# Kernel optimization log

Hardware: AMD Instinct MI355X
Metric: run time of the kernel (lower is better)

## Reference

```python
import jax, jax.numpy as jnp
import numpy as np

N = 65536      # total atoms
D = 1024       # hidden_size (encoder output dim)
H = 2048       # ffn_hidden_size
OUT = 1        # output_size
M = 4096       # number of molecules (segments)


def _lin(k, fi, fo):
    return jax.random.normal(k, (fi, fo), jnp.float32) * (1.0 / np.sqrt(fi))


def setup_inputs() -> dict:
    key = jax.random.key(0)
    ks = jax.random.split(key, 14)
    hidden = jax.random.normal(ks[0], (N, D), jnp.float32)
    segment_ids = jnp.sort(jax.random.randint(ks[1], (N,), 0, M)).astype(jnp.int64)
    inp = {
        "hidden": hidden,
        "ffn_W1": _lin(ks[2], D, H), "ffn_b1": jnp.zeros((H,), jnp.float32),
        "ffn_W2": _lin(ks[3], H, H), "ffn_b2": jnp.zeros((H,), jnp.float32),
        "ffn_W3": _lin(ks[4], H, OUT), "ffn_b3": jnp.zeros((OUT,), jnp.float32),
        "wr_W1": _lin(ks[5], D, H), "wr_b1": jnp.zeros((H,), jnp.float32),
        "wr_W2": _lin(ks[6], H, H), "wr_b2": jnp.zeros((H,), jnp.float32),
        "wr_W3": _lin(ks[7], H, OUT), "wr_b3": jnp.ones((OUT,), jnp.float32),  # bias=1 keeps segment weight sums away from 0
        "segment_ids": segment_ids,
    }
    return inp


def _ffn(x, W1, b1, W2, b2, W3, b3):
    # Dropout(p) is identity in eval; activation = ReLU
    h = jax.nn.relu(x @ W1 + b1)
    h = jax.nn.relu(h @ W2 + b2)
    return h @ W3 + b3


def reference(hidden, ffn_W1, ffn_b1, ffn_W2, ffn_b2, ffn_W3, ffn_b3,
              wr_W1, wr_b1, wr_W2, wr_b2, wr_W3, wr_b3, segment_ids):
    seg = segment_ids.astype(jnp.int32)
    output = _ffn(hidden, ffn_W1, ffn_b1, ffn_W2, ffn_b2, ffn_W3, ffn_b3)   # [N, OUT]
    weights = _ffn(hidden, wr_W1, wr_b1, wr_W2, wr_b2, wr_W3, wr_b3)        # [N, OUT]
    # per-molecule sums over ALL elements of the segment slice (matches .sum())
    out_sum = jax.ops.segment_sum(output.sum(-1), seg, num_segments=M)      # [M]
    w_sum = jax.ops.segment_sum(weights.sum(-1), seg, num_segments=M)       # [M]
    ratio = (out_sum / w_sum)[seg][:, None]                                 # [N, 1]
    return output - weights * ratio
```

## Files before the change

### kernel.cpp

```cpp
#include <hip/hip_runtime.h>
#include <hip/hip_bf16.h>

#define DEVINL __device__ __forceinline__

typedef __attribute__((ext_vector_type(8))) short s8v;
typedef __attribute__((ext_vector_type(4))) float f4v;

using bf16 = __hip_bfloat16;
typedef unsigned short u16;

DEVINL u16 f2bu(float f) {
  bf16 h = __float2bfloat16(f);
  return *reinterpret_cast<u16*>(&h);
}

DEVINL void gload16(const void* g, void* l) {
  __builtin_amdgcn_global_load_lds((const __attribute__((address_space(1))) void*)g,
                                   (__attribute__((address_space(3))) void*)l, 16, 0, 0);
}

#define BAR()    __builtin_amdgcn_s_barrier()
#define LGKM(n)  asm volatile("s_waitcnt lgkmcnt(" #n ")" ::: "memory")
#define VM(n)    asm volatile("s_waitcnt vmcnt(" #n ")" ::: "memory")

__global__ void k_f32_to_bf16(const float* __restrict__ x, u16* __restrict__ y, long n4) {
  long i = (long)blockIdx.x * blockDim.x + threadIdx.x;
  if (i >= n4) return;
  float4 v = ((const float4*)x)[i];
  ushort4 o;
  o.x = f2bu(v.x); o.y = f2bu(v.y); o.z = f2bu(v.z); o.w = f2bu(v.w);
  ((ushort4*)y)[i] = o;
}

__global__ void k_transpose_bf16(const float* __restrict__ W, u16* __restrict__ Wt,
                                 int rows, int cols) {
  __shared__ float tile[32][33];
  const int tx = threadIdx.x, ty = threadIdx.y;
  const int c0 = blockIdx.x * 32, r0 = blockIdx.y * 32;
  #pragma unroll
  for (int i = ty; i < 32; i += 8)
    tile[i][tx] = W[(long)(r0 + i) * cols + (c0 + tx)];
  __syncthreads();
  #pragma unroll
  for (int i = ty; i < 32; i += 8)
    Wt[(long)(c0 + i) * rows + (r0 + tx)] = f2bu(tile[tx][i]);
}

extern __shared__ char smem[];

template<int EPI, int NT>
__global__ __launch_bounds__(512, 2)
void k_gemm8(const u16* __restrict__ A, const u16* __restrict__ Bt,
             u16* __restrict__ C, const float* __restrict__ bias,
             const float* __restrict__ w3, float* __restrict__ oacc,
             int N, int K) {
  const int tid = threadIdx.x;
  const int w = tid >> 6, lane = tid & 63;
  const int id = blockIdx.x;
  const int cpx = gridDim.x >> 3;
  const int sw = (id & 7) * cpx + (id >> 3);
  const int bn = sw & 7, bm = sw >> 3;

  const int wm = (w >> 2) * 128, wn = (w & 3) * 64;

  f4v acc[8][4];
  #pragma unroll
  for (int i = 0; i < 8; ++i)
    #pragma unroll
    for (int jj = 0; jj < 4; ++jj)
      #pragma unroll
      for (int r = 0; r < 4; ++r) acc[i][jj][r] = 0.f;

  const int rowl = tid >> 2;
  const int jsw = (tid & 3) ^ ((rowl >> 1) & 3);
  const u16* gA = A + (long)(bm * 256 + rowl) * K + jsw * 8;
  const u16* gB = Bt + (long)(bn * 256 + rowl) * K + jsw * 8;
  const long cstr = (long)128 * K;
  const uint wb = (uint)w * 1024u;

  const uint swz = ((uint)((lane >> 4) ^ ((lane >> 1) & 3))) * 16u;
  const uint aoff = (uint)(wm + (lane & 15)) * 64u + swz;
  const uint boff = (uint)(wn + (lane & 15)) * 64u + swz + 32768u;

#define STAGE_A(pp, ks, rel) do { \
    const u16* g_ = gA + (rel) * 64 + (ks) * 32; \
    char* l_ = smem + (uint)(pp) * 65536u + (uint)(ks) * 16384u + wb; \
    gload16(g_, l_); gload16(g_ + cstr, l_ + 8192); } while (0)
#define STAGE_B(pp, ks, rel) do { \
    const u16* g_ = gB + (rel) * 64 + (ks) * 32; \
    char* l_ = smem + (uint)(pp) * 65536u + 32768u + (uint)(ks) * 16384u + wb; \
    gload16(g_, l_); gload16(g_ + cstr, l_ + 8192); } while (0)

#define RD_A(dst, pbc, ksb) do { \
    _Pragma("unroll") \
    for (int mi_ = 0; mi_ < 8; ++mi_) \
      dst[mi_] = *(const s8v*)(smem + (pbc) + (ksb) + aoff + (uint)mi_ * 1024u); } while (0)
#define RD_B(dst, pbc, ksb, c0) do { \
    dst[0] = *(const s8v*)(smem + (pbc) + (ksb) + boff + (uint)(c0) * 1024u); \
    dst[1] = *(const s8v*)(smem + (pbc) + (ksb) + boff + (uint)((c0) + 1) * 1024u); } while (0)

#define MFMA8(A_, B_, c0i, c1i) do { \
    __builtin_amdgcn_s_setprio(1); \
    _Pragma("unroll") \
    for (int mi_ = 0; mi_ < 8; ++mi_) { \
      acc[mi_][c0i] = __builtin_amdgcn_mfma_f32_16x16x32_bf16(A_[mi_], B_[0], acc[mi_][c0i], 0, 0, 0); \
      acc[mi_][c1i] = __builtin_amdgcn_mfma_f32_16x16x32_bf16(A_[mi_], B_[1], acc[mi_][c1i], 0, 0, 0); \
    } \
    __builtin_amdgcn_s_setprio(0); } while (0)

#define TILE(P, REL1, REL2, S1, S2, R1) do { \
     \
    RD_B(b23, (P) * 65536u, 0u, 2); \
    if (S1) STAGE_A(1 - (P), 1, REL1); \
    BAR(); LGKM(2); \
    MFMA8(a0, b01, 0, 1); \
     \
    if (S1) { VM(6); } else { VM(0); } \
    BAR(); \
    RD_A(a1, (P) * 65536u, 16384u); RD_B(b01, (P) * 65536u, 16384u, 0); \
    if (S1) STAGE_B(1 - (P), 1, REL1); \
    LGKM(10); \
    MFMA8(a0, b23, 2, 3); \
     \
    RD_B(b23, (P) * 65536u, 16384u, 2); \
    if (S2) STAGE_A((P), 0, REL2); \
    BAR(); LGKM(2); \
    MFMA8(a1, b01, 0, 1); \
     \
    if (S2) { \
      STAGE_B((P), 0, REL2); \
      VM(8); BAR(); \
      RD_A(a0, (1 - (P)) * 65536u, 0u); RD_B(b01, (1 - (P)) * 65536u, 0u, 0); \
      LGKM(10); \
    } else if (R1) { \
      VM(4); BAR(); \
      RD_A(a0, (1 - (P)) * 65536u, 0u); RD_B(b01, (1 - (P)) * 65536u, 0u, 0); \
      LGKM(10); \
    } else { \
      BAR(); LGKM(0); \
    } \
    MFMA8(a1, b23, 2, 3); \
  } while (0)

  s8v a0[8], a1[8], b01[2], b23[2];

  STAGE_A(0, 0, 0); STAGE_B(0, 0, 0); STAGE_A(0, 1, 0); STAGE_B(0, 1, 0);
  STAGE_A(1, 0, 1); STAGE_B(1, 0, 1);
  VM(8); BAR();
  RD_A(a0, 0u, 0u); RD_B(b01, 0u, 0u, 0);

  #pragma unroll 1
  for (int tp = 0; tp < NT / 2 - 1; ++tp) {
    TILE(0, 1, 2, 1, 1, 1);
    TILE(1, 2, 3, 1, 1, 1);
    gA += 128; gB += 128;
  }
  TILE(0, 1, 2, 1, 0, 1);
  TILE(1, 2, 3, 0, 0, 0);

  const int crow = bm * 256 + wm + ((lane >> 4) << 2);
  const int ccol = bn * 256 + wn + (lane & 15);
  if (EPI == 1) {
    #pragma unroll
    for (int jj = 0; jj < 4; ++jj) {
      const float bb = bias[ccol + jj * 16];
      #pragma unroll
      for (int mi = 0; mi < 8; ++mi)
        #pragma unroll
        for (int r = 0; r < 4; ++r) {
          float v = acc[mi][jj][r] + bb;
          v = v > 0.f ? v : 0.f;
          C[(long)(crow + mi * 16 + r) * N + ccol + jj * 16] = f2bu(v);
        }
    }
  } else {
    float bb[4], ww[4];
    #pragma unroll
    for (int jj = 0; jj < 4; ++jj) { bb[jj] = bias[ccol + jj * 16]; ww[jj] = w3[ccol + jj * 16]; }
    #pragma unroll
    for (int mi = 0; mi < 8; ++mi)
      #pragma unroll
      for (int r = 0; r < 4; ++r) {
        float s = 0.f;
        #pragma unroll
        for (int jj = 0; jj < 4; ++jj) {
          float v = acc[mi][jj][r] + bb[jj];
          v = v > 0.f ? v : 0.f;
          s += v * ww[jj];
        }
        s += __shfl_xor(s, 1, 64);
        s += __shfl_xor(s, 2, 64);
        s += __shfl_xor(s, 4, 64);
        s += __shfl_xor(s, 8, 64);
        if ((lane & 15) == 0) atomicAdd(&oacc[crow + mi * 16 + r], s);
      }
  }
#undef STAGE_A
#undef STAGE_B
#undef RD_A
#undef RD_B
#undef MFMA8
#undef TILE
}

__global__ void k_detect(const int* __restrict__ seg, int n, int* __restrict__ flag) {
  if (blockIdx.x == 0 && threadIdx.x == 0) flag[0] = (seg[n - 1] == 0) ? 1 : 0;
}

__global__ void k_segsum(const float* __restrict__ oacc, const float* __restrict__ wacc,
                         const int* __restrict__ seg, const int* __restrict__ flag,
                         const float* __restrict__ ob3, const float* __restrict__ wb3,
                         float* __restrict__ osum, float* __restrict__ wsum, int n) {
  int i = blockIdx.x * blockDim.x + threadIdx.x;
  if (i >= n) return;
  int s = flag[0] ? seg[2 * i] : seg[i];
  atomicAdd(&osum[s], oacc[i] + ob3[0]);
  atomicAdd(&wsum[s], wacc[i] + wb3[0]);
}

__global__ void k_final(const float* __restrict__ oacc, const float* __restrict__ wacc,
                        const int* __restrict__ seg, const int* __restrict__ flag,
                        const float* __restrict__ ob3, const float* __restrict__ wb3,
                        const float* __restrict__ osum, const float* __restrict__ wsum,
                        float* __restrict__ out, int n) {
  int i = blockIdx.x * blockDim.x + threadIdx.x;
  if (i >= n) return;
  int s = flag[0] ? seg[2 * i] : seg[i];
  float o = oacc[i] + ob3[0];
  float ww = wacc[i] + wb3[0];
  out[i] = o - ww * (osum[s] / wsum[s]);
}

extern "C" void kernel_launch(void* const* d_in, const int* in_sizes, int n_in,
                              void* d_out, int out_size, void* d_ws, size_t ws_size,
                              hipStream_t stream) {
  constexpr int NA = 65536, D = 1024, H = 2048, M = 4096;
  const float* hidden = (const float*)d_in[0];
  const float* fW1 = (const float*)d_in[1];
  const float* fb1 = (const float*)d_in[2];
  const float* fW2 = (const float*)d_in[3];
  const float* fb2 = (const float*)d_in[4];
  const float* fW3 = (const float*)d_in[5];
  const float* fb3 = (const float*)d_in[6];
  const float* wW1 = (const float*)d_in[7];
  const float* wb1 = (const float*)d_in[8];
  const float* wW2 = (const float*)d_in[9];
  const float* wb2 = (const float*)d_in[10];
  const float* wW3 = (const float*)d_in[11];
  const float* wb3 = (const float*)d_in[12];
  const int* seg = (const int*)d_in[13];
  float* out = (float*)d_out;

  char* ws = (char*)d_ws;
  size_t off = 0;
  auto alloc = [&](size_t bytes) { char* p = ws + off; off += (bytes + 255) & ~(size_t)255; return p; };
  u16* hbf  = (u16*)alloc((size_t)NA * D * 2);
  u16* w1tf = (u16*)alloc((size_t)H * D * 2);
  u16* w1tw = (u16*)alloc((size_t)H * D * 2);
  u16* w2tf = (u16*)alloc((size_t)H * H * 2);
  u16* w2tw = (u16*)alloc((size_t)H * H * 2);
  u16* h1   = (u16*)alloc((size_t)NA * H * 2);
  float* oacc = (float*)alloc((size_t)NA * 4);
  float* wacc = (float*)alloc((size_t)NA * 4);
  float* osum = (float*)alloc((size_t)M * 4);
  float* wsum = (float*)alloc((size_t)M * 4);
  int* flag = (int*)alloc(256);

  hipFuncSetAttribute((const void*)k_gemm8<1, 16>, hipFuncAttributeMaxDynamicSharedMemorySize, 131072);
  hipFuncSetAttribute((const void*)k_gemm8<2, 32>, hipFuncAttributeMaxDynamicSharedMemorySize, 131072);

  k_f32_to_bf16<<<(int)((long)NA * D / 4 / 256), 256, 0, stream>>>(hidden, hbf, (long)NA * D / 4);
  dim3 tb(32, 8);
  k_transpose_bf16<<<dim3(H / 32, D / 32), tb, 0, stream>>>(fW1, w1tf, D, H);
  k_transpose_bf16<<<dim3(H / 32, D / 32), tb, 0, stream>>>(wW1, w1tw, D, H);
  k_transpose_bf16<<<dim3(H / 32, H / 32), tb, 0, stream>>>(fW2, w2tf, H, H);
  k_transpose_bf16<<<dim3(H / 32, H / 32), tb, 0, stream>>>(wW2, w2tw, H, H);

  hipMemsetAsync(oacc, 0, (size_t)((char*)flag - (char*)oacc), stream);
  k_detect<<<1, 64, 0, stream>>>(seg, NA, flag);

  const int nblk = (H / 256) * (NA / 256);
  k_gemm8<1, 16><<<nblk, 512, 131072, stream>>>(hbf, w1tf, h1, fb1, nullptr, nullptr, H, D);
  k_gemm8<2, 32><<<nblk, 512, 131072, stream>>>(h1, w2tf, nullptr, fb2, fW3, oacc, H, H);
  k_gemm8<1, 16><<<nblk, 512, 131072, stream>>>(hbf, w1tw, h1, wb1, nullptr, nullptr, H, D);
  k_gemm8<2, 32><<<nblk, 512, 131072, stream>>>(h1, w2tw, nullptr, wb2, wW3, wacc, H, H);

  k_segsum<<<NA / 256, 256, 0, stream>>>(oacc, wacc, seg, flag, fb3, wb3, osum, wsum, NA);
  k_final<<<NA / 256, 256, 0, stream>>>(oacc, wacc, seg, flag, fb3, wb3, osum, wsum, out, NA);
}
```

Measured before the change: 1.919 ms.

## Switch GEMM inner loop to 32x32x16 bf16 MFMA with new LDS fragment layout

Replaces the 16x16x32 MFMA tiling with 32x32x16 MFMAs, so each wave holds 4x2 accumulators of 16 floats instead of 8x4 of 4. The LDS read pattern and swizzle offsets are rebuilt for 32-row fragments, and some barriers in the pipelined tile schedule are dropped. The epilogues are remapped to the 32x32 output layout, and the row reduction gains an extra shuffle. The aim is fewer MFMA issues and fewer LDS fragment reads per FLOP, at the cost of a different pipeline and barrier schedule that may race or stall.

```diff
diff --git a/kernel.cpp b/kernel.cpp
--- a/kernel.cpp
+++ b/kernel.cpp
@@ -4,7 +4,7 @@
 #define DEVINL __device__ __forceinline__
 
 typedef __attribute__((ext_vector_type(8))) short s8v;
-typedef __attribute__((ext_vector_type(4))) float f4v;
+typedef __attribute__((ext_vector_type(16))) float f16v;
 
 using bf16 = __hip_bfloat16;
 typedef unsigned short u16;
@@ -63,13 +63,13 @@
 
   const int wm = (w >> 2) * 128, wn = (w & 3) * 64;
 
-  f4v acc[8][4];
-  #pragma unroll
-  for (int i = 0; i < 8; ++i)
-    #pragma unroll
-    for (int jj = 0; jj < 4; ++jj)
+  f16v acc[4][2];
+  #pragma unroll
+  for (int mi = 0; mi < 4; ++mi)
+    #pragma unroll
+    for (int ni = 0; ni < 2; ++ni)
       #pragma unroll
-      for (int r = 0; r < 4; ++r) acc[i][jj][r] = 0.f;
+      for (int r = 0; r < 16; ++r) acc[mi][ni][r] = 0.f;
 
   const int rowl = tid >> 2;
   const int jsw = (tid & 3) ^ ((rowl >> 1) & 3);
@@ -78,9 +78,14 @@
   const long cstr = (long)128 * K;
   const uint wb = (uint)w * 1024u;
 
-  const uint swz = ((uint)((lane >> 4) ^ ((lane >> 1) & 3))) * 16u;
-  const uint aoff = (uint)(wm + (lane & 15)) * 64u + swz;
-  const uint boff = (uint)(wn + (lane & 15)) * 64u + swz + 32768u;
+  const uint arow = (uint)(wm + (lane & 31)) * 64u;
+  const uint brow = (uint)(wn + (lane & 31)) * 64u + 32768u;
+  const uint hi = (uint)((lane >> 5) & 1);
+  const uint xw = (uint)((lane >> 1) & 3);
+  uint sl[4];
+  #pragma unroll
+  for (int s = 0; s < 4; ++s)
+    sl[s] = (((uint)(2 * (s & 1)) + hi) ^ xw) * 16u + (uint)(s >> 1) * 16384u;
 
 #define STAGE_A(pp, ks, rel) do { \
     const u16* g_ = gA + (rel) * 64 + (ks) * 32; \
@@ -91,63 +96,63 @@
     char* l_ = smem + (uint)(pp) * 65536u + 32768u + (uint)(ks) * 16384u + wb; \
     gload16(g_, l_); gload16(g_ + cstr, l_ + 8192); } while (0)
 
-#define RD_A(dst, pbc, ksb) do { \
-    _Pragma("unroll") \
-    for (int mi_ = 0; mi_ < 8; ++mi_) \
-      dst[mi_] = *(const s8v*)(smem + (pbc) + (ksb) + aoff + (uint)mi_ * 1024u); } while (0)
-#define RD_B(dst, pbc, ksb, c0) do { \
-    dst[0] = *(const s8v*)(smem + (pbc) + (ksb) + boff + (uint)(c0) * 1024u); \
-    dst[1] = *(const s8v*)(smem + (pbc) + (ksb) + boff + (uint)((c0) + 1) * 1024u); } while (0)
-
-#define MFMA8(A_, B_, c0i, c1i) do { \
+#define RD6(aD, bD, pbc, s) do { \
+    aD[0] = *(const s8v*)(smem + (pbc) + arow + sl[s]); \
+    aD[1] = *(const s8v*)(smem + (pbc) + arow + sl[s] + 2048u); \
+    aD[2] = *(const s8v*)(smem + (pbc) + arow + sl[s] + 4096u); \
+    aD[3] = *(const s8v*)(smem + (pbc) + arow + sl[s] + 6144u); \
+    bD[0] = *(const s8v*)(smem + (pbc) + brow + sl[s]); \
+    bD[1] = *(const s8v*)(smem + (pbc) + brow + sl[s] + 2048u); } while (0)
+
+#define MFMA8(aS, bS) do { \
     __builtin_amdgcn_s_setprio(1); \
     _Pragma("unroll") \
-    for (int mi_ = 0; mi_ < 8; ++mi_) { \
-      acc[mi_][c0i] = __builtin_amdgcn_mfma_f32_16x16x32_bf16(A_[mi_], B_[0], acc[mi_][c0i], 0, 0, 0); \
-      acc[mi_][c1i] = __builtin_amdgcn_mfma_f32_16x16x32_bf16(A_[mi_], B_[1], acc[mi_][c1i], 0, 0, 0); \
+    for (int mi_ = 0; mi_ < 4; ++mi_) { \
+      acc[mi_][0] = __builtin_amdgcn_mfma_f32_32x32x16_bf16(aS[mi_], bS[0], acc[mi_][0], 0, 0, 0); \
+      acc[mi_][1] = __builtin_amdgcn_mfma_f32_32x32x16_bf16(aS[mi_], bS[1], acc[mi_][1], 0, 0, 0); \
     } \
     __builtin_amdgcn_s_setprio(0); } while (0)
 
 #define TILE(P, REL1, REL2, S1, S2, R1) do { \
      \
-    RD_B(b23, (P) * 65536u, 0u, 2); \
+    RD6(aY, bY, (P) * 65536u, 1); \
     if (S1) STAGE_A(1 - (P), 1, REL1); \
-    BAR(); LGKM(2); \
-    MFMA8(a0, b01, 0, 1); \
+    LGKM(6); \
+    MFMA8(aX, bX); \
      \
     if (S1) { VM(6); } else { VM(0); } \
     BAR(); \
-    RD_A(a1, (P) * 65536u, 16384u); RD_B(b01, (P) * 65536u, 16384u, 0); \
+    RD6(aX, bX, (P) * 65536u, 2); \
     if (S1) STAGE_B(1 - (P), 1, REL1); \
-    LGKM(10); \
-    MFMA8(a0, b23, 2, 3); \
-     \
-    RD_B(b23, (P) * 65536u, 16384u, 2); \
+    LGKM(6); \
+    MFMA8(aY, bY); \
+     \
+    RD6(aY, bY, (P) * 65536u, 3); \
     if (S2) STAGE_A((P), 0, REL2); \
-    BAR(); LGKM(2); \
-    MFMA8(a1, b01, 0, 1); \
+    LGKM(6); \
+    MFMA8(aX, bX); \
      \
     if (S2) { \
+      VM(6); BAR(); \
+      RD6(aX, bX, (1 - (P)) * 65536u, 0); \
       STAGE_B((P), 0, REL2); \
-      VM(8); BAR(); \
-      RD_A(a0, (1 - (P)) * 65536u, 0u); RD_B(b01, (1 - (P)) * 65536u, 0u, 0); \
-      LGKM(10); \
+      LGKM(6); \
     } else if (R1) { \
       VM(4); BAR(); \
-      RD_A(a0, (1 - (P)) * 65536u, 0u); RD_B(b01, (1 - (P)) * 65536u, 0u, 0); \
-      LGKM(10); \
+      RD6(aX, bX, (1 - (P)) * 65536u, 0); \
+      LGKM(6); \
     } else { \
-      BAR(); LGKM(0); \
+      LGKM(0); \
     } \
-    MFMA8(a1, b23, 2, 3); \
+    MFMA8(aY, bY); \
   } while (0)
 
-  s8v a0[8], a1[8], b01[2], b23[2];
+  s8v aX[4], aY[4], bX[2], bY[2];
 
   STAGE_A(0, 0, 0); STAGE_B(0, 0, 0); STAGE_A(0, 1, 0); STAGE_B(0, 1, 0);
   STAGE_A(1, 0, 1); STAGE_B(1, 0, 1);
   VM(8); BAR();
-  RD_A(a0, 0u, 0u); RD_B(b01, 0u, 0u, 0);
+  RD6(aX, bX, 0u, 0);
 
   #pragma unroll 1
   for (int tp = 0; tp < NT / 2 - 1; ++tp) {
@@ -158,47 +163,50 @@
   TILE(0, 1, 2, 1, 0, 1);
   TILE(1, 2, 3, 0, 0, 0);
 
-  const int crow = bm * 256 + wm + ((lane >> 4) << 2);
-  const int ccol = bn * 256 + wn + (lane & 15);
+  const int colb = bn * 256 + wn + (lane & 31);
+  const int rowb = bm * 256 + wm + 4 * ((lane >> 5) & 1);
   if (EPI == 1) {
     #pragma unroll
-    for (int jj = 0; jj < 4; ++jj) {
-      const float bb = bias[ccol + jj * 16];
+    for (int ni = 0; ni < 2; ++ni) {
+      const int col = colb + ni * 32;
+      const float bb = bias[col];
       #pragma unroll
-      for (int mi = 0; mi < 8; ++mi)
+      for (int mi = 0; mi < 4; ++mi)
         #pragma unroll
-        for (int r = 0; r < 4; ++r) {
-          float v = acc[mi][jj][r] + bb;
+        for (int r = 0; r < 16; ++r) {
+          const int row = rowb + mi * 32 + (r & 3) + 8 * (r >> 2);
+          float v = acc[mi][ni][r] + bb;
           v = v > 0.f ? v : 0.f;
-          C[(long)(crow + mi * 16 + r) * N + ccol + jj * 16] = f2bu(v);
+          C[(long)row * N + col] = f2bu(v);
         }
     }
   } else {
-    float bb[4], ww[4];
-    #pragma unroll
-    for (int jj = 0; jj < 4; ++jj) { bb[jj] = bias[ccol + jj * 16]; ww[jj] = w3[ccol + jj * 16]; }
-    #pragma unroll
-    for (int mi = 0; mi < 8; ++mi)
+    float bb[2], ww[2];
+    #pragma unroll
+    for (int ni = 0; ni < 2; ++ni) { bb[ni] = bias[colb + ni * 32]; ww[ni] = w3[colb + ni * 32]; }
+    #pragma unroll
+    for (int mi = 0; mi < 4; ++mi)
       #pragma unroll
-      for (int r = 0; r < 4; ++r) {
+      for (int r = 0; r < 16; ++r) {
         float s = 0.f;
         #pragma unroll
-        for (int jj = 0; jj < 4; ++jj) {
-          float v = acc[mi][jj][r] + bb[jj];
+        for (int ni = 0; ni < 2; ++ni) {
+          float v = acc[mi][ni][r] + bb[ni];
           v = v > 0.f ? v : 0.f;
-          s += v * ww[jj];
+          s += v * ww[ni];
         }
         s += __shfl_xor(s, 1, 64);
         s += __shfl_xor(s, 2, 64);
         s += __shfl_xor(s, 4, 64);
         s += __shfl_xor(s, 8, 64);
-        if ((lane & 15) == 0) atomicAdd(&oacc[crow + mi * 16 + r], s);
+        s += __shfl_xor(s, 16, 64);
+        if ((lane & 31) == 0)
+          atomicAdd(&oacc[rowb + mi * 32 + (r & 3) + 8 * (r >> 2)], s);
       }
   }
 #undef STAGE_A
 #undef STAGE_B
-#undef RD_A
-#undef RD_B
+#undef RD6
 #undef MFMA8
 #undef TILE
 }
```

After: 2.312 ms. 20.4% more time.

## Load GEMM B fragments directly from global into registers, drop B LDS staging

Applied to the files above, without the earlier changes.

The GEMM kernel no longer stages the weight (B) tiles through shared memory. Each lane loads its B MFMA fragments straight from global memory into registers, double-buffered across k-steps, while A stays staged in LDS. This halves LDS usage to 64KB, which could allow more blocks per CU, and removes LDS traffic for B. The cost is uncoalesced, redundant global/L2 reads of B (each wave fetches its own 64 columns) and a reworked vmcnt schedule that has to cover both the B register loads and the A LDS loads.

```diff
diff --git a/kernel.cpp b/kernel.cpp
--- a/kernel.cpp
+++ b/kernel.cpp
@@ -20,7 +20,6 @@
 }
 
 #define BAR()    __builtin_amdgcn_s_barrier()
-#define LGKM(n)  asm volatile("s_waitcnt lgkmcnt(" #n ")" ::: "memory")
 #define VM(n)    asm volatile("s_waitcnt vmcnt(" #n ")" ::: "memory")
 
 __global__ void k_f32_to_bf16(const float* __restrict__ x, u16* __restrict__ y, long n4) {
@@ -74,30 +73,28 @@
   const int rowl = tid >> 2;
   const int jsw = (tid & 3) ^ ((rowl >> 1) & 3);
   const u16* gA = A + (long)(bm * 256 + rowl) * K + jsw * 8;
-  const u16* gB = Bt + (long)(bn * 256 + rowl) * K + jsw * 8;
   const long cstr = (long)128 * K;
   const uint wb = (uint)w * 1024u;
 
   const uint swz = ((uint)((lane >> 4) ^ ((lane >> 1) & 3))) * 16u;
   const uint aoff = (uint)(wm + (lane & 15)) * 64u + swz;
-  const uint boff = (uint)(wn + (lane & 15)) * 64u + swz + 32768u;
+
+  const u16* gBf = Bt + (long)(bn * 256 + wn + (lane & 15)) * K + ((lane >> 4) & 3) * 8;
+  const long nstr = (long)16 * K;
 
 #define STAGE_A(pp, ks, rel) do { \
     const u16* g_ = gA + (rel) * 64 + (ks) * 32; \
-    char* l_ = smem + (uint)(pp) * 65536u + (uint)(ks) * 16384u + wb; \
-    gload16(g_, l_); gload16(g_ + cstr, l_ + 8192); } while (0)
-#define STAGE_B(pp, ks, rel) do { \
-    const u16* g_ = gB + (rel) * 64 + (ks) * 32; \
-    char* l_ = smem + (uint)(pp) * 65536u + 32768u + (uint)(ks) * 16384u + wb; \
+    char* l_ = smem + (uint)(pp) * 32768u + (uint)(ks) * 16384u + wb; \
     gload16(g_, l_); gload16(g_ + cstr, l_ + 8192); } while (0)
 
 #define RD_A(dst, pbc, ksb) do { \
     _Pragma("unroll") \
     for (int mi_ = 0; mi_ < 8; ++mi_) \
       dst[mi_] = *(const s8v*)(smem + (pbc) + (ksb) + aoff + (uint)mi_ * 1024u); } while (0)
-#define RD_B(dst, pbc, ksb, c0) do { \
-    dst[0] = *(const s8v*)(smem + (pbc) + (ksb) + boff + (uint)(c0) * 1024u); \
-    dst[1] = *(const s8v*)(smem + (pbc) + (ksb) + boff + (uint)((c0) + 1) * 1024u); } while (0)
+
+#define LD_B(dst, koff, c0) do { \
+    dst[0] = *(const s8v*)(gBf + (koff) + (c0) * nstr); \
+    dst[1] = *(const s8v*)(gBf + (koff) + ((c0) + 1) * nstr); } while (0)
 
 #define MFMA8(A_, B_, c0i, c1i) do { \
     __builtin_amdgcn_s_setprio(1); \
@@ -108,55 +105,41 @@
     } \
     __builtin_amdgcn_s_setprio(0); } while (0)
 
-#define TILE(P, REL1, REL2, S1, S2, R1) do { \
-     \
-    RD_B(b23, (P) * 65536u, 0u, 2); \
+#define TILE(P, REL1, REL2, S1, S2, R1, BL2, KO1, KO2, G2N, G4N) do { \
+     \
     if (S1) STAGE_A(1 - (P), 1, REL1); \
-    BAR(); LGKM(2); \
-    MFMA8(a0, b01, 0, 1); \
-     \
-    if (S1) { VM(6); } else { VM(0); } \
-    BAR(); \
-    RD_A(a1, (P) * 65536u, 16384u); RD_B(b01, (P) * 65536u, 16384u, 0); \
-    if (S1) STAGE_B(1 - (P), 1, REL1); \
-    LGKM(10); \
-    MFMA8(a0, b23, 2, 3); \
-     \
-    RD_B(b23, (P) * 65536u, 16384u, 2); \
+    LD_B(bk1a, KO1, 0); \
+    MFMA8(a0, bk0a, 0, 1); \
+     \
+    LD_B(bk1b, KO1, 2); \
+    VM(G2N); BAR(); \
+    RD_A(a1, (P) * 32768u, 16384u); \
+    MFMA8(a0, bk0b, 2, 3); \
+     \
     if (S2) STAGE_A((P), 0, REL2); \
-    BAR(); LGKM(2); \
-    MFMA8(a1, b01, 0, 1); \
-     \
-    if (S2) { \
-      STAGE_B((P), 0, REL2); \
-      VM(8); BAR(); \
-      RD_A(a0, (1 - (P)) * 65536u, 0u); RD_B(b01, (1 - (P)) * 65536u, 0u, 0); \
-      LGKM(10); \
-    } else if (R1) { \
-      VM(4); BAR(); \
-      RD_A(a0, (1 - (P)) * 65536u, 0u); RD_B(b01, (1 - (P)) * 65536u, 0u, 0); \
-      LGKM(10); \
-    } else { \
-      BAR(); LGKM(0); \
-    } \
-    MFMA8(a1, b23, 2, 3); \
+    if (BL2) LD_B(bk0a, KO2, 0); \
+    MFMA8(a1, bk1a, 0, 1); \
+     \
+    if (BL2) LD_B(bk0b, KO2, 2); \
+    if (R1) { VM(G4N); BAR(); RD_A(a0, (1 - (P)) * 32768u, 0u); } \
+    MFMA8(a1, bk1b, 2, 3); \
   } while (0)
 
-  s8v a0[8], a1[8], b01[2], b23[2];
-
-  STAGE_A(0, 0, 0); STAGE_B(0, 0, 0); STAGE_A(0, 1, 0); STAGE_B(0, 1, 0);
-  STAGE_A(1, 0, 1); STAGE_B(1, 0, 1);
-  VM(8); BAR();
-  RD_A(a0, 0u, 0u); RD_B(b01, 0u, 0u, 0);
+  s8v a0[8], a1[8], bk0a[2], bk0b[2], bk1a[2], bk1b[2];
+
+  STAGE_A(0, 0, 0); STAGE_A(0, 1, 0); STAGE_A(1, 0, 1);
+  LD_B(bk0a, 0, 0); LD_B(bk0b, 0, 2);
+  VM(4); BAR();
+  RD_A(a0, 0u, 0u);
 
   #pragma unroll 1
   for (int tp = 0; tp < NT / 2 - 1; ++tp) {
-    TILE(0, 1, 2, 1, 1, 1);
-    TILE(1, 2, 3, 1, 1, 1);
-    gA += 128; gB += 128;
+    TILE(0, 1, 2, 1, 1, 1, 1, 32, 64, 16, 16);
+    TILE(1, 2, 3, 1, 1, 1, 1, 96, 128, 16, 16);
+    gA += 128; gBf += 128;
   }
-  TILE(0, 1, 2, 1, 0, 1);
-  TILE(1, 2, 3, 0, 0, 0);
+  TILE(0, 1, 2, 1, 0, 1, 1, 32, 64, 16, 14);
+  TILE(1, 2, 3, 0, 0, 0, 0, 96, 128, 12, 0);
 
   const int crow = bm * 256 + wm + ((lane >> 4) << 2);
   const int ccol = bn * 256 + wn + (lane & 15);
@@ -196,9 +179,8 @@
       }
   }
 #undef STAGE_A
-#undef STAGE_B
 #undef RD_A
-#undef RD_B
+#undef LD_B
 #undef MFMA8
 #undef TILE
 }
@@ -266,8 +248,8 @@
   float* wsum = (float*)alloc((size_t)M * 4);
   int* flag = (int*)alloc(256);
 
-  hipFuncSetAttribute((const void*)k_gemm8<1, 16>, hipFuncAttributeMaxDynamicSharedMemorySize, 131072);
-  hipFuncSetAttribute((const void*)k_gemm8<2, 32>, hipFuncAttributeMaxDynamicSharedMemorySize, 131072);
+  hipFuncSetAttribute((const void*)k_gemm8<1, 16>, hipFuncAttributeMaxDynamicSharedMemorySize, 65536);
+  hipFuncSetAttribute((const void*)k_gemm8<2, 32>, hipFuncAttributeMaxDynamicSharedMemorySize, 65536);
 
   k_f32_to_bf16<<<(int)((long)NA * D / 4 / 256), 256, 0, stream>>>(hidden, hbf, (long)NA * D / 4);
   dim3 tb(32, 8);
@@ -280,10 +262,10 @@
   k_detect<<<1, 64, 0, stream>>>(seg, NA, flag);
 
   const int nblk = (H / 256) * (NA / 256);
-  k_gemm8<1, 16><<<nblk, 512, 131072, stream>>>(hbf, w1tf, h1, fb1, nullptr, nullptr, H, D);
-  k_gemm8<2, 32><<<nblk, 512, 131072, stream>>>(h1, w2tf, nullptr, fb2, fW3, oacc, H, H);
-  k_gemm8<1, 16><<<nblk, 512, 131072, stream>>>(hbf, w1tw, h1, wb1, nullptr, nullptr, H, D);
-  k_gemm8<2, 32><<<nblk, 512, 131072, stream>>>(h1, w2tw, nullptr, wb2, wW3, wacc, H, H);
+  k_gemm8<1, 16><<<nblk, 512, 65536, stream>>>(hbf, w1tf, h1, fb1, nullptr, nullptr, H, D);
+  k_gemm8<2, 32><<<nblk, 512, 65536, stream>>>(h1, w2tf, nullptr, fb2, fW3, oacc, H, H);
+  k_gemm8<1, 16><<<nblk, 512, 65536, stream>>>(hbf, w1tw, h1, wb1, nullptr, nullptr, H, D);
+  k_gemm8<2, 32><<<nblk, 512, 65536, stream>>>(h1, w2tw, nullptr, wb2, wW3, wacc, H, H);
 
   k_segsum<<<NA / 256, 256, 0, stream>>>(oacc, wacc, seg, flag, fb3, wb3, osum, wsum, NA);
   k_final<<<NA / 256, 256, 0, stream>>>(oacc, wacc, seg, flag, fb3, wb3, osum, wsum, out, NA);
```

Result: slower. 2.549 ms (+32.8%).
